# Optimization experiments

Hardware: AMD Instinct MI355X
Metric: run time of the kernel (lower is better)

The kernel has to match this reference:

```python
import jax, jax.numpy as jnp
import numpy as np

C = 256          # n_channels
D = 32           # head_dim
HEADS = C // D   # 8 heads in the MLA block
EXP = 4          # MBConv expansion
EPS = 1e-15      # attention epsilon
BN_EPS = 1e-5    # BatchNorm eps (eval mode, mean=0, var=1)
BN_SCALE = 1.0 / np.sqrt(1.0 + BN_EPS)


def _hswish(x):
    return x * jnp.clip(x + 3.0, 0.0, 6.0) * (1.0 / 6.0)


def _dwconv(x, w, pad):
    # depthwise conv, NCHW, weight (Cout,1,k,k), groups = Cout
    return jax.lax.conv_general_dilated(
        x, w, (1, 1), [(pad, pad), (pad, pad)],
        feature_group_count=w.shape[0],
        dimension_numbers=('NCHW', 'OIHW', 'NCHW'))


def _bn(x, gamma, beta):
    # eval-mode BN with running_mean=0, running_var=1
    return (gamma * BN_SCALE)[None, :, None, None] * x + beta[None, :, None, None]


def setup_inputs() -> dict:
    key = jax.random.key(0)
    ks = jax.random.split(key, 16)
    s = 0.05
    return {
        'x': jax.random.normal(ks[0], (8, C, 64, 64), jnp.float32),
        'W_qkv': jax.random.normal(ks[1], (3 * C, C), jnp.float32) * s,
        'W_dw5': jax.random.normal(ks[2], (3 * C, 1, 5, 5), jnp.float32) * s,
        'W_pw': jax.random.normal(ks[3], (3 * HEADS, D, D), jnp.float32) * s,
        'W_proj': jax.random.normal(ks[4], (C, 2 * C), jnp.float32) * s,
        'g_proj': jnp.ones((C,), jnp.float32),
        'b_proj': jnp.zeros((C,), jnp.float32),
        'W_e': jax.random.normal(ks[5], (EXP * C, C), jnp.float32) * s,
        'b_e': jax.random.normal(ks[6], (EXP * C,), jnp.float32) * s,
        'W_dw3': jax.random.normal(ks[7], (EXP * C, 1, 3, 3), jnp.float32) * s,
        'b_dw3': jax.random.normal(ks[8], (EXP * C,), jnp.float32) * s,
        'W_p': jax.random.normal(ks[9], (C, EXP * C), jnp.float32) * s,
        'g_p': jnp.ones((C,), jnp.float32),
        'b_p': jnp.zeros((C,), jnp.float32),
    }


def reference(x, W_qkv, W_dw5, W_pw, W_proj, g_proj, b_proj,
              W_e, b_e, W_dw3, b_dw3, W_p, g_p, b_p):
    B, _, H, W = x.shape
    # --- LightweightMLABlock ---
    qkv = jnp.einsum('oi,bihw->bohw', W_qkv, x)                 # (B,3C,H,W)
    # multi-scale aggregator: dw5x5 -> grouped 1x1 (groups=3*HEADS, 32x32 each)
    ag = _dwconv(qkv, W_dw5, 2)
    ag = ag.reshape(B, 3 * HEADS, D, H, W)
    ag = jnp.einsum('ged,bgdhw->bgehw', W_pw, ag).reshape(B, 3 * C, H, W)
    qkv_cat = jnp.concatenate([qkv, ag], axis=1)                # (B,6C,H,W)
    # ReLU linear attention (H*W=4096 > D=32 -> linear branch)
    N = H * W
    t = qkv_cat.reshape(B, 2 * HEADS, 3 * D, N)
    q = jax.nn.relu(t[:, :, :D])
    k = jax.nn.relu(t[:, :, D:2 * D])
    v = t[:, :, 2 * D:]
    vpad = jnp.concatenate([v, jnp.ones((B, 2 * HEADS, 1, N), v.dtype)], axis=2)
    vk = jnp.einsum('bhdn,bhen->bhde', vpad, k)                 # (B,h,D+1,D)
    out = jnp.einsum('bhde,bhen->bhdn', vk, q)                  # (B,h,D+1,N)
    out = out[:, :, :D] / (out[:, :, D:] + EPS)
    att = out.reshape(B, 2 * C, H, W)
    proj = _bn(jnp.einsum('oi,bihw->bohw', W_proj, att), g_proj, b_proj)
    y = proj + x                                                # attention residual
    # --- MobileBottleneckBlock ---
    e = _hswish(jnp.einsum('oi,bihw->bohw', W_e, y) + b_e[None, :, None, None])
    d = _hswish(_dwconv(e, W_dw3, 1) + b_dw3[None, :, None, None])
    p = _bn(jnp.einsum('oi,bihw->bohw', W_p, d), g_p, b_p)
    return p + y                                                # MBConv residual
```

## Files before the change

### kernel.cpp

```cpp
#include <hip/hip_runtime.h>

typedef __bf16 bf16;
typedef __attribute__((ext_vector_type(8))) __bf16 bf16x8;
typedef __attribute__((ext_vector_type(4))) __bf16 bf16x4;
typedef __attribute__((ext_vector_type(2))) __bf16 bf16x2;
typedef __attribute__((ext_vector_type(4))) float f32x4;
typedef __attribute__((ext_vector_type(2))) float f32x2;

static constexpr int NPIX = 4096;
static constexpr float BN_SC = 0.9999950000374997f;
static constexpr float ATT_EPS = 1e-15f;

__device__ __forceinline__ float hswish_f(float v) {
  return v * fminf(fmaxf(v + 3.0f, 0.0f), 6.0f) * (1.0f / 6.0f);
}

__device__ __forceinline__ void gload16(const void* g, void* l) {
  __builtin_amdgcn_global_load_lds(
      (const __attribute__((address_space(1))) unsigned int*)g,
      (__attribute__((address_space(3))) unsigned int*)l, 16, 0, 0);
}

__device__ __forceinline__ float b2f_lo(unsigned int u) {
  union { unsigned int i; float f; } v; v.i = u << 16; return v.f;
}
__device__ __forceinline__ float b2f_hi(unsigned int u) {
  union { unsigned int i; float f; } v; v.i = u & 0xffff0000u; return v.f;
}
__device__ __forceinline__ unsigned short f2b_u(float f) {
  union { float f; unsigned int i; } v; v.f = f;
  unsigned int r = v.i + 0x7FFFu + ((v.i >> 16) & 1u);
  return (unsigned short)(r >> 16);
}
__device__ __forceinline__ unsigned int relu2(unsigned int v) {
  const unsigned int s = v & 0x80008000u;
  const unsigned int m = (s >> 15) * 0xFFFFu;
  return v & ~m;
}

__global__ __launch_bounds__(256)
void x_to_nhwc(const float* __restrict__ x, bf16* __restrict__ xn) {
  __shared__ float t[32][65];
  const int img = blockIdx.z;
  const int n0 = blockIdx.x * 64, c0 = blockIdx.y * 32;
  const int tid = threadIdx.x;
  const float* xb = x + ((size_t)img * 256 + c0) * NPIX + n0;
  {
    const int col = tid & 63, r0 = tid >> 6;
#pragma unroll
    for (int i = 0; i < 8; ++i) {
      const int r = r0 + i * 4;
      t[r][col] = xb[(size_t)r * NPIX + col];
    }
  }
  __syncthreads();
  const int n = tid & 63, cq = tid >> 6;
  bf16x8 v;
#pragma unroll
  for (int j = 0; j < 8; ++j) v[j] = (bf16)t[cq * 8 + j][n];
  *(bf16x8*)(xn + ((size_t)img * NPIX + n0 + n) * 256 + c0 + cq * 8) = v;
}

__global__ void wcvt3(const float* __restrict__ W_proj, const float* __restrict__ W_e,
                      const float* __restrict__ W_p, bf16* __restrict__ o_proj,
                      bf16* __restrict__ o_e, bf16* __restrict__ o_p) {
  const int i = blockIdx.x * 256 + threadIdx.x;
  if (i < 131072) o_proj[i] = (bf16)W_proj[i];
  else if (i < 393216) o_e[i - 131072] = (bf16)W_e[i - 131072];
  else o_p[i - 393216] = (bf16)W_p[i - 393216];
}

__global__ void wqkv_perm(const float* __restrict__ w, bf16* __restrict__ o) {
  const int row = blockIdx.x;
  const int t = row >> 8, r = row & 255, h = r >> 5, d = r & 31;
  const int oldrow = h * 96 + t * 32 + d;
  o[row * 256 + threadIdx.x] = (bf16)w[oldrow * 256 + threadIdx.x];
}

template<int EPI>
__global__ __launch_bounds__(256, 3)
void mfma_gemm(const bf16* __restrict__ A, const bf16* __restrict__ Bact,
               bf16* __restrict__ Yb, float* __restrict__ Yf,
               const int M, const int K,
               const float* __restrict__ p0, const float* __restrict__ p1,
               const bf16* __restrict__ res)
{
  __shared__ __attribute__((aligned(16))) char ldsA[16384];
  __shared__ __attribute__((aligned(16))) char ldsB[16384];
  const int img = blockIdx.z;
  const int n0 = blockIdx.x * 128;
  const int m0 = blockIdx.y * 128;
  const bf16* Bi = Bact + (size_t)img * NPIX * K;
  const int tid = threadIdx.x;
  const int w = tid >> 6, l = tid & 63;
  const int g = l >> 4, ln = l & 15;
  const int wr = w >> 1, wc = w & 1;
  const int lrow = l >> 3;
  const int sofs = (((l & 7) ^ lrow) << 4);

  f32x4 acc[4][4];
#pragma unroll
  for (int i = 0; i < 4; ++i)
#pragma unroll
    for (int j = 0; j < 4; ++j) acc[i][j] = (f32x4){0.f, 0.f, 0.f, 0.f};

  const char* Abase = (const char*)(A + (size_t)m0 * K);
  const char* Bbase = (const char*)(Bi + (size_t)n0 * K);
  const size_t rowb = (size_t)K * 2;
  const int swz = (ln & 7) << 4;

  const int nk = K >> 6;
  for (int kt = 0; kt < nk; ++kt) {
    const int k0b = kt << 7;
#pragma unroll
    for (int i = 0; i < 4; ++i) {
      const int q = (w << 2) + i;
      const int r = q * 8 + lrow;
      gload16(Abase + (size_t)r * rowb + k0b + sofs, ldsA + q * 1024);
    }
#pragma unroll
    for (int i = 0; i < 4; ++i) {
      const int q = (w << 2) + i;
      const int r = q * 8 + lrow;
      gload16(Bbase + (size_t)r * rowb + k0b + sofs, ldsB + q * 1024);
    }
    __syncthreads();
#pragma unroll
    for (int kk = 0; kk < 2; ++kk) {
      bf16x8 av[4], bv[4];
#pragma unroll
      for (int f = 0; f < 4; ++f) {
        const int ra = wr * 64 + f * 16 + ln;
        const int rb = wc * 64 + f * 16 + ln;
        const int kb = kk * 64 + (g << 4);
        av[f] = *(const bf16x8*)(ldsA + ra * 128 + (kb ^ swz));
        bv[f] = *(const bf16x8*)(ldsB + rb * 128 + (kb ^ swz));
      }
#pragma unroll
      for (int fi = 0; fi < 4; ++fi)
#pragma unroll
        for (int fj = 0; fj < 4; ++fj)
          acc[fi][fj] = __builtin_amdgcn_mfma_f32_16x16x32_bf16(
              av[fi], bv[fj], acc[fi][fj], 0, 0, 0);
    }
    __syncthreads();
  }

#pragma unroll
  for (int fi = 0; fi < 4; ++fi) {
    const int m4 = m0 + wr * 64 + fi * 16 + g * 4;
    f32x4 P0 = {0.f, 0.f, 0.f, 0.f}, P1 = {0.f, 0.f, 0.f, 0.f};
    if (EPI == 1 || EPI == 3) { P0 = *(const f32x4*)(p0 + m4); P1 = *(const f32x4*)(p1 + m4); }
    if (EPI == 2) { P0 = *(const f32x4*)(p0 + m4); }
#pragma unroll
    for (int fj = 0; fj < 4; ++fj) {
      const int n = n0 + wc * 64 + fj * 16 + ln;
      if (EPI == 3) {
        const bf16x4 yr = *(const bf16x4*)(res + ((size_t)img * NPIX + n) * 256 + m4);
        float* op = Yf + ((size_t)img * 256 + m4) * NPIX + n;
#pragma unroll
        for (int r = 0; r < 4; ++r)
          op[(size_t)r * NPIX] = P0[r] * BN_SC * acc[fi][fj][r] + P1[r] + (float)yr[r];
      } else {
        bf16x4 sv;
        if (EPI == 0) {
#pragma unroll
          for (int r = 0; r < 4; ++r) sv[r] = (bf16)acc[fi][fj][r];
        } else if (EPI == 1) {
          const bf16x4 xr = *(const bf16x4*)(res + ((size_t)img * NPIX + n) * 256 + m4);
#pragma unroll
          for (int r = 0; r < 4; ++r)
            sv[r] = (bf16)(P0[r] * BN_SC * acc[fi][fj][r] + P1[r] + (float)xr[r]);
        } else {
#pragma unroll
          for (int r = 0; r < 4; ++r)
            sv[r] = (bf16)hswish_f(acc[fi][fj][r] + P0[r]);
        }
        *(bf16x4*)(Yb + ((size_t)img * NPIX + n) * M + m4) = sv;
      }
    }
  }
}

__global__ __launch_bounds__(512)
void dw5pw_nhwc(const bf16* __restrict__ qkv, const float* __restrict__ W5,
                const float* __restrict__ Wpw, bf16* __restrict__ ag) {
  const int gch = blockIdx.y, img = blockIdx.z;
  const int t_ = gch >> 3, hh_ = gch & 7;
  const int n0 = blockIdx.x * 256;
  const int r0 = n0 >> 6;
  __shared__ __attribute__((aligned(16))) unsigned int sInT[16 * 548];
  __shared__ __attribute__((aligned(16))) unsigned int sS32[256 * 20];
  __shared__ __attribute__((aligned(16))) bf16 sPw[32 * 32];
  const int tid = threadIdx.x;
  for (int i = tid; i < 1024; i += 512) sPw[i] = (bf16)Wpw[(hh_ * 3 + t_) * 1024 + i];
  for (int i = tid; i < 2176; i += 512) {
    const int s = i & 3, hp = i >> 2;
    const int hr = hp / 68, hc = hp - hr * 68;
    const int gr = r0 + hr - 2, gc = hc - 2;
    uint4 vv = {0u, 0u, 0u, 0u};
    if (gr >= 0 && gr < 64 && gc >= 0 && gc < 64)
      vv = *(const uint4*)(qkv + ((size_t)img * NPIX + gr * 64 + gc) * 768 + gch * 32 + s * 8);
    unsigned int* rp = sInT + (s * 4) * 548 + hp;
    rp[0] = vv.x; rp[548] = vv.y; rp[1096] = vv.z; rp[1644] = vv.w;
  }
  const int ci = tid & 15;
  f32x2 w2[25];
  {
    const float* wp0 = W5 + (size_t)(hh_ * 96 + t_ * 32 + 2 * ci) * 25;
#pragma unroll
    for (int q = 0; q < 25; ++q) w2[q] = (f32x2){wp0[q], wp0[25 + q]};
  }
  __syncthreads();
  {
    const int pg = tid >> 4;
    const int p0 = pg * 8;
    const int prow = p0 >> 6, pcol = p0 & 63;
    f32x2 a2[8];
#pragma unroll
    for (int px = 0; px < 8; ++px) a2[px] = (f32x2){0.f, 0.f};
#pragma unroll
    for (int ky = 0; ky < 5; ++ky) {
      const unsigned int* wp = &sInT[ci * 548 + (prow + ky) * 68 + pcol];
      const uint4 qa = *(const uint4*)wp;
      const uint4 qb = *(const uint4*)(wp + 4);
      const uint4 qc = *(const uint4*)(wp + 8);
      const unsigned int win[12] = {qa.x, qa.y, qa.z, qa.w, qb.x, qb.y, qb.z, qb.w,
                                    qc.x, qc.y, qc.z, qc.w};
      f32x2 val[12];
#pragma unroll
      for (int j = 0; j < 12; ++j) val[j] = (f32x2){b2f_lo(win[j]), b2f_hi(win[j])};
#pragma unroll
      for (int px = 0; px < 8; ++px)
#pragma unroll
        for (int kx = 0; kx < 5; ++kx)
          a2[px] = val[px + kx] * w2[ky * 5 + kx] + a2[px];
    }
#pragma unroll
    for (int px = 0; px < 8; ++px) {
      const unsigned int pk = (unsigned int)f2b_u(a2[px][0]) | ((unsigned int)f2b_u(a2[px][1]) << 16);
      sS32[(p0 + px) * 20 + ci] = pk;
    }
  }
  __syncthreads();
  {
    const int w = tid >> 6, l = tid & 63;
    const int lg = l >> 4, ln = l & 15;
    f32x4 acc[2][2];
#pragma unroll
    for (int i = 0; i < 2; ++i)
#pragma unroll
      for (int j = 0; j < 2; ++j) acc[i][j] = (f32x4){0.f, 0.f, 0.f, 0.f};
    bf16x8 av[2], bv[2];
#pragma unroll
    for (int et = 0; et < 2; ++et)
      av[et] = *(const bf16x8*)((const char*)sPw + (et * 16 + ln) * 64 + lg * 16);
#pragma unroll
    for (int pt = 0; pt < 2; ++pt)
      bv[pt] = *(const bf16x8*)((const char*)sS32 + ((2 * w + pt) * 16 + ln) * 80 + lg * 16);
#pragma unroll
    for (int et = 0; et < 2; ++et)
#pragma unroll
      for (int pt = 0; pt < 2; ++pt)
        acc[et][pt] = __builtin_amdgcn_mfma_f32_16x16x32_bf16(av[et], bv[pt], acc[et][pt], 0, 0, 0);
#pragma unroll
    for (int et = 0; et < 2; ++et)
#pragma unroll
      for (int pt = 0; pt < 2; ++pt) {
        const int e0 = et * 16 + lg * 4;
        const int p = n0 + (2 * w + pt) * 16 + ln;
        bf16x4 sv;
#pragma unroll
        for (int r = 0; r < 4; ++r) sv[r] = (bf16)acc[et][pt][r];
        *(bf16x4*)(ag + ((size_t)img * NPIX + p) * 768 + gch * 32 + e0) = sv;
      }
  }
}

__global__ __launch_bounds__(256)
void vk_part(const bf16* __restrict__ qkv, const bf16* __restrict__ ag,
             float* __restrict__ partial) {
  const int chunk = blockIdx.x, src = blockIdx.y, img = blockIdx.z;
  const bf16* base = (src == 0 ? qkv : ag) + (size_t)img * NPIX * 768 + 256;
  __shared__ __attribute__((aligned(16))) char tile[32 * 1024];
  const int tid = threadIdx.x;
  const int h = tid >> 5;
  const int r5 = tid & 31;
  const int et = r5 & 3;
  const int dq = r5 >> 2;
  const int spx = tid >> 3, sseg = tid & 7;
  f32x2 acc[4][4];
#pragma unroll
  for (int i = 0; i < 4; ++i)
#pragma unroll
    for (int j = 0; j < 4; ++j) acc[i][j] = (f32x2){0.f, 0.f};
  f32x2 dsum[4] = {(f32x2){0.f,0.f},(f32x2){0.f,0.f},(f32x2){0.f,0.f},(f32x2){0.f,0.f}};
  for (int sub = 0; sub < 2; ++sub) {
    __syncthreads();
    {
      const int px0 = chunk * 64 + sub * 32;
      const char* gp = (const char*)(base + (size_t)(px0 + spx) * 768) + sseg * 128;
      char* lp = tile + spx * 1024;
      const int swz = (spx & 7) << 4;
#pragma unroll
      for (int i = 0; i < 8; ++i) {
        uint4 v = *(const uint4*)(gp + i * 16);
        if (sseg < 4) {
          v.x = relu2(v.x); v.y = relu2(v.y); v.z = relu2(v.z); v.w = relu2(v.w);
        }
        *(uint4*)(lp + ((sseg * 128 + i * 16) ^ swz)) = v;
      }
    }
    __syncthreads();
    for (int nn = 0; nn < 32; ++nn) {
      const char* row = tile + nn * 1024;
      const int swzn = (nn & 7) << 4;
      f32x2 kp[4];
#pragma unroll
      for (int j = 0; j < 4; ++j) {
        const unsigned int kk = *(const unsigned int*)(row + ((h * 64 + (et * 4 + j) * 4) ^ swzn));
        kp[j] = (f32x2){b2f_lo(kk), b2f_hi(kk)};
      }
      const unsigned int v0 = *(const unsigned int*)(row + ((512 + h * 64 + dq * 8) ^ swzn));
      const unsigned int v1 = *(const unsigned int*)(row + ((512 + h * 64 + dq * 8 + 4) ^ swzn));
      const float vd[4] = {b2f_lo(v0), b2f_hi(v0), b2f_lo(v1), b2f_hi(v1)};
#pragma unroll
      for (int i = 0; i < 4; ++i)
#pragma unroll
        for (int j = 0; j < 4; ++j)
          acc[i][j] = (f32x2){vd[i], vd[i]} * kp[j] + acc[i][j];
      if (dq == 0) {
#pragma unroll
        for (int j = 0; j < 4; ++j) dsum[j] = dsum[j] + kp[j];
      }
    }
  }
  float* pb = partial + ((size_t)((img * 2 + src) * 64 + chunk)) * 8448;
#pragma unroll
  for (int i = 0; i < 4; ++i) {
    const int d = dq * 4 + i;
#pragma unroll
    for (int j = 0; j < 4; ++j) {
      pb[h * 1056 + d * 32 + et * 8 + j * 2]     = acc[i][j][0];
      pb[h * 1056 + d * 32 + et * 8 + j * 2 + 1] = acc[i][j][1];
    }
  }
  if (dq == 0) {
#pragma unroll
    for (int j = 0; j < 4; ++j) {
      pb[h * 1056 + 1024 + et * 8 + j * 2]     = dsum[j][0];
      pb[h * 1056 + 1024 + et * 8 + j * 2 + 1] = dsum[j][1];
    }
  }
}

__global__ __launch_bounds__(256)
void vk_reduce(const float* __restrict__ partial, bf16* __restrict__ svkT,
               float* __restrict__ dvec) {
  const int h = blockIdx.x & 15, img = blockIdx.x >> 4;
  const int tid = threadIdx.x;
  const int e = tid & 31, dq = tid >> 5;
  const int src = h >> 3, hh = h & 7;
  const float* pb = partial + (size_t)((img * 2 + src) * 64) * 8448 + hh * 1056;
  float a[4] = {};
  for (int c = 0; c < 64; ++c) {
    const float* pc = pb + (size_t)c * 8448;
#pragma unroll
    for (int j = 0; j < 4; ++j) a[j] += pc[(dq * 4 + j) * 32 + e];
  }
  bf16x4 o;
#pragma unroll
  for (int j = 0; j < 4; ++j) o[j] = (bf16)a[j];
  *(bf16x4*)(svkT + (((size_t)img * 16 + h) * 32 + e) * 32 + dq * 4) = o;
  if (dq == 0) {
    float ds = 0.f;
    for (int c = 0; c < 64; ++c) ds += pb[(size_t)c * 8448 + 1024 + e];
    dvec[((size_t)img * 16 + h) * 32 + e] = ds;
  }
}

__global__ __launch_bounds__(256)
void att_pix(const bf16* __restrict__ qkv, const bf16* __restrict__ ag,
             const bf16* __restrict__ svkT, const float* __restrict__ dvec,
             bf16* __restrict__ att) {
  const int pc = blockIdx.x;
  const int img = blockIdx.z;
  __shared__ __attribute__((aligned(16))) unsigned int squ[16][264];
  __shared__ __attribute__((aligned(16))) bf16 ssvk[16 * 1024];
  __shared__ float sdv[512];
  const int tid = threadIdx.x;
  const int px0 = pc * 16;
  const int px = tid >> 4, s = tid & 15;
  {
    const bf16* srcp = (s < 8 ? qkv : ag) + (size_t)(img * NPIX + px0 + px) * 768 + (s & 7) * 32;
#pragma unroll
    for (int i = 0; i < 4; ++i) {
      uint4 v = *(const uint4*)((const char*)srcp + i * 16);
      v.x = relu2(v.x); v.y = relu2(v.y); v.z = relu2(v.z); v.w = relu2(v.w);
      *(uint4*)&squ[px][s * 16 + i * 4] = v;
    }
  }
  {
    const bf16* sb = svkT + (size_t)img * 16384;
    for (int i = tid; i < 2048; i += 256)
      *(bf16x8*)(ssvk + i * 8) = *(const bf16x8*)(sb + i * 8);
    const float* db = dvec + (size_t)img * 512;
    for (int i = tid; i < 512; i += 256) sdv[i] = db[i];
  }
  __syncthreads();
  const int sd = s, d0 = sd * 2;
  const unsigned int* sv32 = (const unsigned int*)ssvk;
  bf16* ob = att + (size_t)(img * NPIX + px0 + px) * 512;
#pragma unroll
  for (int h = 0; h < 16; ++h) {
    const unsigned int* qp = &squ[px][h * 16];
    const unsigned int* kp = sv32 + h * 512 + sd;
    const float* dp = &sdv[h * 32];
    float a0 = 0.f, a1 = 0.f, den = 0.f;
#pragma unroll
    for (int e2 = 0; e2 < 16; ++e2) {
      const unsigned int qq = qp[e2];
      const float q0 = b2f_lo(qq), q1 = b2f_hi(qq);
      const unsigned int w0 = kp[(2 * e2) * 16];
      const unsigned int w1 = kp[(2 * e2 + 1) * 16];
      a0 = fmaf(q0, b2f_lo(w0), a0); a0 = fmaf(q1, b2f_lo(w1), a0);
      a1 = fmaf(q0, b2f_hi(w0), a1); a1 = fmaf(q1, b2f_hi(w1), a1);
      den = fmaf(q0, dp[2 * e2], den); den = fmaf(q1, dp[2 * e2 + 1], den);
    }
    const float inv = 1.f / (den + ATT_EPS);
    bf16x2 o; o[0] = (bf16)(a0 * inv); o[1] = (bf16)(a1 * inv);
    *(bf16x2*)(ob + h * 32 + d0) = o;
  }
}

__global__ __launch_bounds__(256)
void dw3_nhwc(const bf16* __restrict__ ein, const float* __restrict__ w3,
              const float* __restrict__ bias, bf16* __restrict__ dout) {
  const int idx = blockIdx.x * 256 + threadIdx.x;
  const int c8 = idx & 127;
  const int seg = idx >> 7;
  const int img = seg >> 8;
  const int p0 = (seg & 255) * 16;
  const int ch = c8 * 8;
  float wr_[9][8];
#pragma unroll
  for (int j = 0; j < 8; ++j)
#pragma unroll
    for (int q = 0; q < 9; ++q) wr_[q][j] = w3[(ch + j) * 9 + q];
  const f32x4 b0 = *(const f32x4*)(bias + ch), b1 = *(const f32x4*)(bias + ch + 4);
  const int row = p0 >> 6, col0 = p0 & 63;
  const bf16* ib = ein + (size_t)img * NPIX * 1024 + ch;
  bf16* ob = dout + (size_t)img * NPIX * 1024 + ch;
  for (int pp = 0; pp < 16; ++pp) {
    const int col = col0 + pp;
    float a[8] = {b0[0], b0[1], b0[2], b0[3], b1[0], b1[1], b1[2], b1[3]};
#pragma unroll
    for (int ky = 0; ky < 3; ++ky) {
      const int r = row + ky - 1;
      if (r < 0 || r > 63) continue;
#pragma unroll
      for (int kx = 0; kx < 3; ++kx) {
        const int cc = col + kx - 1;
        if (cc < 0 || cc > 63) continue;
        const bf16x8 v = *(const bf16x8*)(ib + (size_t)(r * 64 + cc) * 1024);
#pragma unroll
        for (int j = 0; j < 8; ++j) a[j] += wr_[ky * 3 + kx][j] * (float)v[j];
      }
    }
    bf16x8 o;
#pragma unroll
    for (int j = 0; j < 8; ++j) o[j] = (bf16)hswish_f(a[j]);
    *(bf16x8*)(ob + (size_t)(row * 64 + col) * 1024) = o;
  }
}

extern "C" void kernel_launch(void* const* d_in, const int* in_sizes, int n_in,
                              void* d_out, int out_size, void* d_ws, size_t ws_size,
                              hipStream_t stream) {
  const float* x      = (const float*)d_in[0];
  const float* W_qkv  = (const float*)d_in[1];
  const float* W_dw5  = (const float*)d_in[2];
  const float* W_pw   = (const float*)d_in[3];
  const float* W_proj = (const float*)d_in[4];
  const float* g_proj = (const float*)d_in[5];
  const float* b_proj = (const float*)d_in[6];
  const float* W_e    = (const float*)d_in[7];
  const float* b_e    = (const float*)d_in[8];
  const float* W_dw3  = (const float*)d_in[9];
  const float* b_dw3  = (const float*)d_in[10];
  const float* W_p    = (const float*)d_in[11];
  const float* g_p    = (const float*)d_in[12];
  const float* b_p    = (const float*)d_in[13];
  float* out = (float*)d_out;

  int nb = 8;
  while (nb > 1) {
    size_t need = (size_t)nb * 25331712ull + 1703936ull + 1024;
    if (need <= ws_size) break;
    nb >>= 1;
  }

  char* p = (char*)d_ws;
  float* partial = (float*)p;                 p += (size_t)nb * 4325376;
  float* dvec    = (float*)p;                 p += (size_t)nb * 2048;
  bf16* wq_bf    = (bf16*)p;                  p += 196608ull * 2;
  bf16* wproj_bf = (bf16*)p;                  p += 131072ull * 2;
  bf16* we_bf    = (bf16*)p;                  p += 262144ull * 2;
  bf16* wp_bf    = (bf16*)p;                  p += 262144ull * 2;
  bf16* svkT     = (bf16*)p;                  p += (size_t)nb * 32768;
  bf16* arena    = (bf16*)p;
  bf16* xn   = arena;
  bf16* qkvb = arena + (size_t)nb * 1048576;
  bf16* agb  = qkvb + (size_t)nb * 3145728;
  bf16* attb = agb + (size_t)nb * 3145728;
  bf16* yb   = attb + (size_t)nb * 2097152;
  bf16* eb   = qkvb;
  bf16* db   = qkvb + (size_t)nb * 4194304;

  wqkv_perm<<<768, 256, 0, stream>>>(W_qkv, wq_bf);
  wcvt3<<<2560, 256, 0, stream>>>(W_proj, W_e, W_p, wproj_bf, we_bf, wp_bf);

  for (int b0 = 0; b0 < 8; b0 += nb) {
    const float* x_c = x + (size_t)b0 * 256 * NPIX;
    float* out_c = out + (size_t)b0 * 256 * NPIX;

    x_to_nhwc<<<dim3(64, 8, nb), 256, 0, stream>>>(x_c, xn);
    mfma_gemm<0><<<dim3(32, 6, nb), 256, 0, stream>>>(wq_bf, xn, qkvb, nullptr,
                                                      768, 256, nullptr, nullptr, nullptr);
    dw5pw_nhwc<<<dim3(16, 24, nb), 512, 0, stream>>>(qkvb, W_dw5, W_pw, agb);
    vk_part<<<dim3(64, 2, nb), 256, 0, stream>>>(qkvb, agb, partial);
    vk_reduce<<<nb * 16, 256, 0, stream>>>(partial, svkT, dvec);
    att_pix<<<dim3(256, 1, nb), 256, 0, stream>>>(qkvb, agb, svkT, dvec, attb);
    mfma_gemm<1><<<dim3(32, 2, nb), 256, 0, stream>>>(wproj_bf, attb, yb, nullptr,
                                                      256, 512, g_proj, b_proj, xn);
    mfma_gemm<2><<<dim3(32, 8, nb), 256, 0, stream>>>(we_bf, yb, eb, nullptr,
                                                      1024, 256, b_e, nullptr, nullptr);
    dw3_nhwc<<<nb * 128, 256, 0, stream>>>(eb, W_dw3, b_dw3, db);
    mfma_gemm<3><<<dim3(32, 2, nb), 256, 0, stream>>>(wp_bf, db, nullptr, out_c,
                                                      256, 1024, g_p, b_p, yb);
  }
}
```

Measured before the change: 365.3 us.

## Restructure depthwise 3x3 conv as column-wise sliding row window with register reuse

The depthwise 3x3 kernel is remapped so each block handles one image column over 16 rows, with each thread owning 4 channels. Input rows are kept in a rotating three-row register window, so each input pixel is loaded once per column instead of nine times. The multiply-adds use packed f32x2 operations. The cost is narrower 8-byte loads per thread and a different grid shape, which may change coalescing and occupancy.

```diff
diff --git a/kernel.cpp b/kernel.cpp
--- a/kernel.cpp
+++ b/kernel.cpp
@@ -433,44 +433,60 @@
   }
 }
 
+#define DW3_LOADROW(r, sl)                                                     \
+  {                                                                            \
+    for (int cs = 0; cs < 3; ++cs) {                                           \
+      const int cc = col + cs - 1;                                             \
+      if ((unsigned)(r) < 64u && (unsigned)cc < 64u) {                         \
+        const uint2 v = *(const uint2*)(ib + (size_t)((r) * 64 + cc) * 1024);  \
+        rr[sl][cs][0] = (f32x2){b2f_lo(v.x), b2f_hi(v.x)};                     \
+        rr[sl][cs][1] = (f32x2){b2f_lo(v.y), b2f_hi(v.y)};                     \
+      } else {                                                                 \
+        rr[sl][cs][0] = (f32x2){0.f, 0.f};                                     \
+        rr[sl][cs][1] = (f32x2){0.f, 0.f};                                     \
+      }                                                                        \
+    }                                                                          \
+  }
+
 __global__ __launch_bounds__(256)
 void dw3_nhwc(const bf16* __restrict__ ein, const float* __restrict__ w3,
               const float* __restrict__ bias, bf16* __restrict__ dout) {
-  const int idx = blockIdx.x * 256 + threadIdx.x;
-  const int c8 = idx & 127;
-  const int seg = idx >> 7;
-  const int img = seg >> 8;
-  const int p0 = (seg & 255) * 16;
-  const int ch = c8 * 8;
-  float wr_[9][8];
-#pragma unroll
-  for (int j = 0; j < 8; ++j)
-#pragma unroll
-    for (int q = 0; q < 9; ++q) wr_[q][j] = w3[(ch + j) * 9 + q];
-  const f32x4 b0 = *(const f32x4*)(bias + ch), b1 = *(const f32x4*)(bias + ch + 4);
-  const int row = p0 >> 6, col0 = p0 & 63;
+  const int img = blockIdx.z;
+  const int r0 = blockIdx.y * 16;
+  const int col = blockIdx.x;
+  const int tid = threadIdx.x;
+  const int ch = tid * 4;
+  f32x2 wv[9][2];
+#pragma unroll
+  for (int p = 0; p < 2; ++p)
+#pragma unroll
+    for (int q = 0; q < 9; ++q)
+      wv[q][p] = (f32x2){w3[(ch + 2 * p) * 9 + q], w3[(ch + 2 * p + 1) * 9 + q]};
+  f32x2 bv[2];
+  bv[0] = (f32x2){bias[ch], bias[ch + 1]};
+  bv[1] = (f32x2){bias[ch + 2], bias[ch + 3]};
   const bf16* ib = ein + (size_t)img * NPIX * 1024 + ch;
   bf16* ob = dout + (size_t)img * NPIX * 1024 + ch;
-  for (int pp = 0; pp < 16; ++pp) {
-    const int col = col0 + pp;
-    float a[8] = {b0[0], b0[1], b0[2], b0[3], b1[0], b1[1], b1[2], b1[3]};
-#pragma unroll
-    for (int ky = 0; ky < 3; ++ky) {
-      const int r = row + ky - 1;
-      if (r < 0 || r > 63) continue;
-#pragma unroll
-      for (int kx = 0; kx < 3; ++kx) {
-        const int cc = col + kx - 1;
-        if (cc < 0 || cc > 63) continue;
-        const bf16x8 v = *(const bf16x8*)(ib + (size_t)(r * 64 + cc) * 1024);
-#pragma unroll
-        for (int j = 0; j < 8; ++j) a[j] += wr_[ky * 3 + kx][j] * (float)v[j];
-      }
-    }
-    bf16x8 o;
-#pragma unroll
-    for (int j = 0; j < 8; ++j) o[j] = (bf16)hswish_f(a[j]);
-    *(bf16x8*)(ob + (size_t)(row * 64 + col) * 1024) = o;
+  f32x2 rr[3][3][2];
+  DW3_LOADROW(r0 - 1, 0);
+  DW3_LOADROW(r0, 1);
+#pragma unroll
+  for (int i = 0; i < 16; ++i) {
+    const int slm = i % 3, sl0 = (i + 1) % 3, slp = (i + 2) % 3;
+    DW3_LOADROW(r0 + i + 1, slp);
+    f32x2 a[2] = {bv[0], bv[1]};
+#pragma unroll
+    for (int kx = 0; kx < 3; ++kx)
+#pragma unroll
+      for (int p = 0; p < 2; ++p) {
+        a[p] = rr[slm][kx][p] * wv[0 * 3 + kx][p] + a[p];
+        a[p] = rr[sl0][kx][p] * wv[1 * 3 + kx][p] + a[p];
+        a[p] = rr[slp][kx][p] * wv[2 * 3 + kx][p] + a[p];
+      }
+    uint2 o;
+    o.x = (unsigned)f2b_u(hswish_f(a[0][0])) | ((unsigned)f2b_u(hswish_f(a[0][1])) << 16);
+    o.y = (unsigned)f2b_u(hswish_f(a[1][0])) | ((unsigned)f2b_u(hswish_f(a[1][1])) << 16);
+    *(uint2*)(ob + (size_t)((r0 + i) * 64 + col) * 1024) = o;
   }
 }
 
@@ -535,7 +551,7 @@
                                                       256, 512, g_proj, b_proj, xn);
     mfma_gemm<2><<<dim3(32, 8, nb), 256, 0, stream>>>(we_bf, yb, eb, nullptr,
                                                       1024, 256, b_e, nullptr, nullptr);
-    dw3_nhwc<<<nb * 128, 256, 0, stream>>>(eb, W_dw3, b_dw3, db);
+    dw3_nhwc<<<dim3(64, 4, nb), 256, 0, stream>>>(eb, W_dw3, b_dw3, db);
     mfma_gemm<3><<<dim3(32, 2, nb), 256, 0, stream>>>(wp_bf, db, nullptr, out_c,
                                                       256, 1024, g_p, b_p, yb);
   }
```

After: 360.6 us. About the same (-1.3%).
